# Optimization experiments

Hardware: AMD Instinct MI355X
Metric: run time of the kernel (lower is better)

Reference implementation:

```python
import jax, jax.numpy as jnp
import numpy as np

EMBED_DIM = 1024
NUM_HEADS = 16
HEAD_SIZE = EMBED_DIM // NUM_HEADS  # 64
MAX_EMBED_DIM = 2048
MAX_HEAD_SIZE = 128
B, T = 4, 2048


def setup_inputs() -> dict:
    key = jax.random.key(0)
    kx, kq, kk, kv = jax.random.split(key, 4)
    x = jax.random.normal(kx, (B, T, MAX_EMBED_DIM), dtype=jnp.float32)
    # base-head weights sized for the max config; slices are taken in reference()
    Wq = jax.random.normal(kq, (NUM_HEADS, MAX_HEAD_SIZE, MAX_EMBED_DIM), dtype=jnp.float32) * 0.02
    Wk = jax.random.normal(kk, (NUM_HEADS, MAX_HEAD_SIZE, MAX_EMBED_DIM), dtype=jnp.float32) * 0.02
    Wv = jax.random.normal(kv, (NUM_HEADS, MAX_HEAD_SIZE, MAX_EMBED_DIM), dtype=jnp.float32) * 0.02
    return {"x": x, "Wq": Wq, "Wk": Wk, "Wv": Wv}


def reference(x, Wq, Wk, Wv):
    Bx, Tx, _ = x.shape
    xs = x[:, :, :EMBED_DIM]                       # [B, T, E]
    # slice sampled sub-weights: [H, d, E]
    wq = Wq[:, :HEAD_SIZE, :EMBED_DIM]
    wk = Wk[:, :HEAD_SIZE, :EMBED_DIM]
    wv = Wv[:, :HEAD_SIZE, :EMBED_DIM]
    q = jnp.einsum('bte,hde->bhtd', xs, wq)        # [B, H, T, d]
    k = jnp.einsum('bte,hde->bhtd', xs, wk)
    v = jnp.einsum('bte,hde->bhtd', xs, wv)
    scale = jnp.asarray(HEAD_SIZE, x.dtype) ** -0.5
    wei = jnp.einsum('bhtd,bhsd->bhts', q, k) * scale   # [B, H, T, T]
    causal = jnp.tril(jnp.ones((Tx, Tx), dtype=bool))
    wei = jnp.where(causal, wei, jnp.asarray(-jnp.inf, wei.dtype))
    wei = jax.nn.softmax(wei, axis=-1)
    # dropout is identity in eval mode
    out = jnp.einsum('bhts,bhsd->bhtd', wei, v)    # [B, H, T, d]
    out = out.transpose(0, 2, 1, 3).reshape(Bx, Tx, NUM_HEADS * HEAD_SIZE)
    pad = MAX_EMBED_DIM - NUM_HEADS * HEAD_SIZE
    return jnp.pad(out, ((0, 0), (0, 0), (0, pad)))
```

## Files before the change

kernel.cpp:

```cpp
#include <hip/hip_runtime.h>

typedef __attribute__((ext_vector_type(8))) short bf16x8;
typedef __attribute__((ext_vector_type(4))) float f32x4;
typedef __attribute__((ext_vector_type(16))) float f32x16;
typedef __attribute__((ext_vector_type(8))) unsigned short u16x8;
typedef __attribute__((ext_vector_type(4))) unsigned int u32x4;

#define TT 2048

__device__ __forceinline__ unsigned short f2bf(float f) {
  unsigned int u = __builtin_bit_cast(unsigned int, f);
  u += 0x7FFFu + ((u >> 16) & 1u);
  return (unsigned short)(u >> 16);
}

__device__ __forceinline__ void gld16(const void* g, void* l) {
  __builtin_amdgcn_global_load_lds((const __attribute__((address_space(1))) void*)g,
                                   (__attribute__((address_space(3))) void*)l, 16, 0, 0);
}

__device__ __forceinline__ unsigned int cvtpk(float lo, float hi) {
  unsigned int r;
  asm("v_cvt_pk_bf16_f32 %0, %1, %2" : "=v"(r) : "v"(lo), "v"(hi));
  return r;
}

__device__ __forceinline__ void pl32swap(unsigned int& a, unsigned int& b) {
  asm volatile("v_permlane32_swap_b32 %0, %1" : "+v"(a), "+v"(b));
}

__global__ __launch_bounds__(256) void conv_x(const float* __restrict__ x,
                                              unsigned short* __restrict__ xb) {
  const size_t idx = ((size_t)blockIdx.x * 256 + threadIdx.x) * 8;
  const int m = (int)(idx >> 10);
  const int e = (int)(idx & 1023);
  const float4* s = (const float4*)(x + (size_t)m * 2048 + e);
  float4 a = s[0], b = s[1];
  u16x8 v;
  v[0]=f2bf(a.x); v[1]=f2bf(a.y); v[2]=f2bf(a.z); v[3]=f2bf(a.w);
  v[4]=f2bf(b.x); v[5]=f2bf(b.y); v[6]=f2bf(b.z); v[7]=f2bf(b.w);
  *(u16x8*)(xb + idx) = v;
}

__global__ __launch_bounds__(256) void conv_w(const float* __restrict__ Wq,
                                              const float* __restrict__ Wk,
                                              const float* __restrict__ Wv,
                                              unsigned short* __restrict__ wb) {
  const size_t idx = ((size_t)blockIdx.x * 256 + threadIdx.x) * 8;
  const int n = (int)(idx >> 10);
  const int e = (int)(idx & 1023);
  const int mat = n >> 10, hh = (n >> 6) & 15, d = n & 63;
  const float* W = (mat == 0) ? Wq : ((mat == 1) ? Wk : Wv);
  const float4* s = (const float4*)(W + ((size_t)hh * 128 + d) * 2048 + e);
  float4 a = s[0], b = s[1];
  u16x8 v;
  v[0]=f2bf(a.x); v[1]=f2bf(a.y); v[2]=f2bf(a.z); v[3]=f2bf(a.w);
  v[4]=f2bf(b.x); v[5]=f2bf(b.y); v[6]=f2bf(b.z); v[7]=f2bf(b.w);
  *(u16x8*)(wb + idx) = v;
}

__global__ __launch_bounds__(256) void qkv_gemm3(const unsigned short* __restrict__ xb,
                                                 const unsigned short* __restrict__ wb,
                                                 unsigned short* __restrict__ Q,
                                                 unsigned short* __restrict__ Kt,
                                                 unsigned short* __restrict__ Vt) {
  __shared__ unsigned short As[2][128 * 64];
  __shared__ unsigned short Bs[2][128 * 64];
  const int tid = threadIdx.x;
  const int w = tid >> 6, lane = tid & 63, g = lane >> 4, c = lane & 15;
  const int wm = w >> 1, wn = w & 1;
  const int m0 = blockIdx.x * 128;
  const int n0 = blockIdx.y * 128;

  f32x4 acc[4][4];
#pragma unroll
  for (int mi = 0; mi < 4; ++mi)
#pragma unroll
    for (int ni = 0; ni < 4; ++ni) acc[mi][ni] = (f32x4){0.f, 0.f, 0.f, 0.f};

  auto STAGE = [&](int t, int buf) {
    const int k0 = t * 64;
#pragma unroll
    for (int it = 0; it < 4; ++it) {
      const int o = (it * 256 + tid) * 16;
      const int r = o >> 7, cc = o & 127;
      const int cs = cc ^ ((r & 7) << 4);
      gld16(xb + ((size_t)(m0 + r) << 10) + k0 + (cs >> 1), (char*)&As[buf][0] + o);
      gld16(wb + ((size_t)(n0 + r) << 10) + k0 + (cs >> 1), (char*)&Bs[buf][0] + o);
    }
  };

  STAGE(0, 0);
  asm volatile("s_waitcnt vmcnt(0)" ::: "memory");
  __builtin_amdgcn_s_barrier();

  for (int t = 0; t < 16; ++t) {
    const int cur = t & 1;
    if (t + 1 < 16) STAGE(t + 1, cur ^ 1);
#pragma unroll
    for (int kk = 0; kk < 2; ++kk) {
      bf16x8 af[4], bfv[4];
#pragma unroll
      for (int mi = 0; mi < 4; ++mi) {
        const int r = wm * 64 + mi * 16 + c;
        const int cs = (kk * 64 + g * 16) ^ ((r & 7) << 4);
        af[mi] = *(const bf16x8*)((const char*)&As[cur][r * 64] + cs);
      }
#pragma unroll
      for (int ni = 0; ni < 4; ++ni) {
        const int r = wn * 64 + ni * 16 + c;
        const int cs = (kk * 64 + g * 16) ^ ((r & 7) << 4);
        bfv[ni] = *(const bf16x8*)((const char*)&Bs[cur][r * 64] + cs);
      }
      __builtin_amdgcn_s_setprio(1);
#pragma unroll
      for (int mi = 0; mi < 4; ++mi)
#pragma unroll
        for (int ni = 0; ni < 4; ++ni)
          acc[mi][ni] = __builtin_amdgcn_mfma_f32_16x16x32_bf16(af[mi], bfv[ni], acc[mi][ni], 0, 0, 0);
      __builtin_amdgcn_s_setprio(0);
    }
    asm volatile("s_waitcnt vmcnt(0)" ::: "memory");
    __builtin_amdgcn_s_barrier();
  }

#pragma unroll
  for (int mi = 0; mi < 4; ++mi) {
    const int row_l = wm * 64 + mi * 16 + g * 4;
#pragma unroll
    for (int i = 0; i < 4; ++i) {
      const int m = m0 + row_l + i;
      const int b = m >> 11, tt = m & 2047;
#pragma unroll
      for (int ni = 0; ni < 4; ++ni) {
        const int n = n0 + wn * 64 + ni * 16 + c;
        const int mat = n >> 10, hh = (n >> 6) & 15, d = n & 63;
        const unsigned short v = f2bf(acc[mi][ni][i]);
        const size_t bh = (size_t)(b * 16 + hh);
        if (mat == 0)      Q [(bh * TT + tt) * 64 + d] = v;
        else if (mat == 1) Kt[(bh * TT + tt) * 64 + d] = v;
        else               Vt[(bh * 64 + d) * TT + tt] = v;
      }
    }
  }
}

__global__ __launch_bounds__(256) void attn4(const unsigned short* __restrict__ Q,
                                             const unsigned short* __restrict__ K,
                                             const unsigned short* __restrict__ Vt,
                                             float* __restrict__ out) {
  __shared__ unsigned short Ks[2][4096];
  __shared__ unsigned short Vs[2][4096];
  const int blk = blockIdx.x;
  const int bh = blk & 63;
  const int qi = 15 - (blk >> 6);
  const int b = bh >> 4, h = bh & 15;
  const int tid = threadIdx.x;
  const int w = tid >> 6, lane = tid & 63;
  const int ql = lane & 31;
  const int hi = lane >> 5, hi8 = hi * 8;
  const int q0 = qi * 128;
  const int qw = q0 + w * 32;
  const int q = qw + ql;
  const unsigned short* Qp = Q  + (size_t)bh * TT * 64;
  const unsigned short* Kp = K  + (size_t)bh * TT * 64;
  const unsigned short* Vp = Vt + (size_t)bh * 64 * TT;

  bf16x8 qf0, qf1, qf2, qf3;
  {
    const unsigned short* qa = Qp + (size_t)q * 64 + hi8;
    qf0 = *(const bf16x8*)(qa);
    qf1 = *(const bf16x8*)(qa + 16);
    qf2 = *(const bf16x8*)(qa + 32);
    qf3 = *(const bf16x8*)(qa + 48);
  }

  f32x16 o0, o1;
#pragma unroll
  for (int r = 0; r < 16; ++r) { o0[r] = 0.f; o1[r] = 0.f; }
  float m = -3.0e38f, l = 0.f;
  const float c2 = 0.125f * 1.44269504f;

  const int nt = qi * 2 + 2;

  auto STAGE = [&](int t, int buf) {
#pragma unroll
    for (int it = 0; it < 2; ++it) {
      const int o = (it * 256 + tid) * 16;
      const int r = o >> 7, c = o & 127;
      const int cs = c ^ ((r & 7) << 4);
      gld16(Kp + (size_t)t * 4096 + r * 64 + (cs >> 1), (char*)&Ks[buf][0] + o);
      gld16(Vp + (size_t)r * 2048 + t * 64 + (cs >> 1), (char*)&Vs[buf][0] + o);
    }
  };

  STAGE(0, 0);
  asm volatile("s_waitcnt vmcnt(0)" ::: "memory");
  __syncthreads();

  int cur = 0;
  for (int t = 0; t < nt; ++t) {
    if (t + 1 < nt) STAGE(t + 1, cur ^ 1);

#pragma unroll
    for (int s = 0; s < 2; ++s) {
      const int ks32 = t * 64 + s * 32;
      if (ks32 <= qw) {
        const int krow = s * 32 + ql;
        const char* kb = (const char*)&Ks[cur][krow * 64];
        const int ksz = (krow & 7) << 4;
        bf16x8 kf0 = *(const bf16x8*)(kb + ((0  + hi * 16) ^ ksz));
        bf16x8 kf1 = *(const bf16x8*)(kb + ((32 + hi * 16) ^ ksz));
        bf16x8 kf2 = *(const bf16x8*)(kb + ((64 + hi * 16) ^ ksz));
        bf16x8 kf3 = *(const bf16x8*)(kb + ((96 + hi * 16) ^ ksz));
        const int vsz = (ql & 7) << 4;
        const char* vb0 = (const char*)&Vs[cur][ql * 64];
        const char* vb1 = (const char*)&Vs[cur][(ql + 32) * 64];
        bf16x8 vf0 = *(const bf16x8*)(vb0 + ((s * 64 + 0  + hi * 16) ^ vsz));
        bf16x8 vf1 = *(const bf16x8*)(vb0 + ((s * 64 + 32 + hi * 16) ^ vsz));
        bf16x8 vf2 = *(const bf16x8*)(vb1 + ((s * 64 + 0  + hi * 16) ^ vsz));
        bf16x8 vf3 = *(const bf16x8*)(vb1 + ((s * 64 + 32 + hi * 16) ^ vsz));

        f32x16 st;
#pragma unroll
        for (int r = 0; r < 16; ++r) st[r] = 0.f;
        __builtin_amdgcn_s_setprio(1);
        st = __builtin_amdgcn_mfma_f32_32x32x16_bf16(kf0, qf0, st, 0, 0, 0);
        st = __builtin_amdgcn_mfma_f32_32x32x16_bf16(kf1, qf1, st, 0, 0, 0);
        st = __builtin_amdgcn_mfma_f32_32x32x16_bf16(kf2, qf2, st, 0, 0, 0);
        st = __builtin_amdgcn_mfma_f32_32x32x16_bf16(kf3, qf3, st, 0, 0, 0);
        __builtin_amdgcn_s_setprio(0);

        if (ks32 == qw) {
#pragma unroll
          for (int r = 0; r < 16; ++r) {
            const int krw = (r & 3) + 8 * (r >> 2) + 4 * hi;
            if (krw > ql) st[r] = -3.0e38f;
          }
        }

        float t0 = fmaxf(st[0], st[1]),  t1 = fmaxf(st[2], st[3]);
        float t2 = fmaxf(st[4], st[5]),  t3 = fmaxf(st[6], st[7]);
        float t4 = fmaxf(st[8], st[9]),  t5 = fmaxf(st[10], st[11]);
        float t6 = fmaxf(st[12], st[13]), t7 = fmaxf(st[14], st[15]);
        t0 = fmaxf(t0, t1); t2 = fmaxf(t2, t3); t4 = fmaxf(t4, t5); t6 = fmaxf(t6, t7);
        float pm = fmaxf(fmaxf(t0, t2), fmaxf(t4, t6));
        pm = fmaxf(pm, __shfl_xor(pm, 32));
        if (!__all(pm - m <= 44.36f)) {
          const float mnew = fmaxf(m, pm);
          const float alpha = __builtin_amdgcn_exp2f((m - mnew) * c2);
          m = mnew;
          l *= alpha;
#pragma unroll
          for (int r = 0; r < 16; ++r) { o0[r] *= alpha; o1[r] *= alpha; }
        }
        float p[16];
        float rs = 0.f;
#pragma unroll
        for (int r = 0; r < 16; ++r) {
          p[r] = __builtin_amdgcn_exp2f((st[r] - m) * c2);
          rs += p[r];
        }
        rs += __shfl_xor(rs, 32);
        l += rs;

        unsigned int a0 = cvtpk(p[0], p[1]),  a1 = cvtpk(p[2], p[3]);
        unsigned int b0 = cvtpk(p[4], p[5]),  b1 = cvtpk(p[6], p[7]);
        pl32swap(a0, b0); pl32swap(a1, b1);
        unsigned int cc0 = cvtpk(p[8], p[9]),  cc1 = cvtpk(p[10], p[11]);
        unsigned int dd0 = cvtpk(p[12], p[13]), dd1 = cvtpk(p[14], p[15]);
        pl32swap(cc0, dd0); pl32swap(cc1, dd1);
        u32x4 pw0 = {a0, a1, b0, b1};
        u32x4 pw1 = {cc0, cc1, dd0, dd1};
        bf16x8 pf0 = __builtin_bit_cast(bf16x8, pw0);
        bf16x8 pf1 = __builtin_bit_cast(bf16x8, pw1);

        __builtin_amdgcn_s_setprio(1);
        o0 = __builtin_amdgcn_mfma_f32_32x32x16_bf16(vf0, pf0, o0, 0, 0, 0);
        o0 = __builtin_amdgcn_mfma_f32_32x32x16_bf16(vf1, pf1, o0, 0, 0, 0);
        o1 = __builtin_amdgcn_mfma_f32_32x32x16_bf16(vf2, pf0, o1, 0, 0, 0);
        o1 = __builtin_amdgcn_mfma_f32_32x32x16_bf16(vf3, pf1, o1, 0, 0, 0);
        __builtin_amdgcn_s_setprio(0);
      }
    }

    asm volatile("s_waitcnt vmcnt(0)" ::: "memory");
    __syncthreads();
    cur ^= 1;
  }

  const float inv = 1.f / l;
  float* ob = out + ((size_t)b * TT + q) * 2048 + h * 64;
#pragma unroll
  for (int r = 0; r < 16; ++r) {
    const int row = (r & 3) + 8 * (r >> 2) + 4 * hi;
    ob[row]      = o0[r] * inv;
    ob[32 + row] = o1[r] * inv;
  }

  const float4 z = make_float4(0.f, 0.f, 0.f, 0.f);
#pragma unroll
  for (int it = 0; it < 8; ++it) {
    const int idx = it * 256 + tid;
    const int r = idx >> 4, c4 = idx & 15;
    *((float4*)(out + ((size_t)b * TT + q0 + r) * 2048 + 1024 + h * 64) + c4) = z;
  }
}

extern "C" void kernel_launch(void* const* d_in, const int* in_sizes, int n_in,
                              void* d_out, int out_size, void* d_ws, size_t ws_size,
                              hipStream_t stream) {
  const float* x  = (const float*)d_in[0];
  const float* Wq = (const float*)d_in[1];
  const float* Wk = (const float*)d_in[2];
  const float* Wv = (const float*)d_in[3];

  unsigned short* wsp = (unsigned short*)d_ws;
  unsigned short* Q   = wsp;
  unsigned short* Kt  = wsp + (size_t)8388608;
  unsigned short* Vt  = wsp + (size_t)16777216;

  unsigned short* xb = (unsigned short*)d_out;
  unsigned short* wb = (unsigned short*)((char*)d_out + 33554432);
  float* out = (float*)d_out;

  conv_x<<<4096, 256, 0, stream>>>(x, xb);
  conv_w<<<1536, 256, 0, stream>>>(Wq, Wk, Wv, wb);
  qkv_gemm3<<<dim3(64, 24), 256, 0, stream>>>(xb, wb, Q, Kt, Vt);
  attn4<<<1024, 256, 0, stream>>>(Q, Kt, Vt, out);
}
```

Measured before the change: 167.4 us.

## Merge conversion kernels and halve GEMM K-tile to raise occupancy

```diff
diff --git a/kernel.cpp b/kernel.cpp
--- a/kernel.cpp
+++ b/kernel.cpp
@@ -29,64 +29,87 @@
   asm volatile("v_permlane32_swap_b32 %0, %1" : "+v"(a), "+v"(b));
 }
 
-__global__ __launch_bounds__(256) void conv_x(const float* __restrict__ x,
-                                              unsigned short* __restrict__ xb) {
-  const size_t idx = ((size_t)blockIdx.x * 256 + threadIdx.x) * 8;
-  const int m = (int)(idx >> 10);
-  const int e = (int)(idx & 1023);
-  const float4* s = (const float4*)(x + (size_t)m * 2048 + e);
+__global__ __launch_bounds__(256) void conv_all(const float* __restrict__ x,
+                                                const float* __restrict__ Wq,
+                                                const float* __restrict__ Wk,
+                                                const float* __restrict__ Wv,
+                                                unsigned short* __restrict__ xb,
+                                                unsigned short* __restrict__ wb) {
+  const int bid = blockIdx.x;
+  const float* src;
+  unsigned short* dst;
+  size_t idx;
+  if (bid < 4096) {
+    idx = ((size_t)bid * 256 + threadIdx.x) * 8;
+    const int m = (int)(idx >> 10);
+    const int e = (int)(idx & 1023);
+    src = x + (size_t)m * 2048 + e;
+    dst = xb + idx;
+  } else {
+    idx = ((size_t)(bid - 4096) * 256 + threadIdx.x) * 8;
+    const int n = (int)(idx >> 10);
+    const int e = (int)(idx & 1023);
+    const int mat = n >> 10, hh = (n >> 6) & 15, d = n & 63;
+    const float* W = (mat == 0) ? Wq : ((mat == 1) ? Wk : Wv);
+    src = W + ((size_t)hh * 128 + d) * 2048 + e;
+    dst = wb + idx;
+  }
+  const float4* s = (const float4*)src;
   float4 a = s[0], b = s[1];
   u16x8 v;
   v[0]=f2bf(a.x); v[1]=f2bf(a.y); v[2]=f2bf(a.z); v[3]=f2bf(a.w);
   v[4]=f2bf(b.x); v[5]=f2bf(b.y); v[6]=f2bf(b.z); v[7]=f2bf(b.w);
-  *(u16x8*)(xb + idx) = v;
-}
-
-__global__ __launch_bounds__(256) void conv_w(const float* __restrict__ Wq,
-                                              const float* __restrict__ Wk,
-                                              const float* __restrict__ Wv,
-                                              unsigned short* __restrict__ wb) {
-  const size_t idx = ((size_t)blockIdx.x * 256 + threadIdx.x) * 8;
-  const int n = (int)(idx >> 10);
-  const int e = (int)(idx & 1023);
-  const int mat = n >> 10, hh = (n >> 6) & 15, d = n & 63;
-  const float* W = (mat == 0) ? Wq : ((mat == 1) ? Wk : Wv);
-  const float4* s = (const float4*)(W + ((size_t)hh * 128 + d) * 2048 + e);
-  float4 a = s[0], b = s[1];
-  u16x8 v;
-  v[0]=f2bf(a.x); v[1]=f2bf(a.y); v[2]=f2bf(a.z); v[3]=f2bf(a.w);
-  v[4]=f2bf(b.x); v[5]=f2bf(b.y); v[6]=f2bf(b.z); v[7]=f2bf(b.w);
-  *(u16x8*)(wb + idx) = v;
-}
-
-__global__ __launch_bounds__(256) void qkv_gemm3(const unsigned short* __restrict__ xb,
-                                                 const unsigned short* __restrict__ wb,
-                                                 unsigned short* __restrict__ Q,
-                                                 unsigned short* __restrict__ Kt,
-                                                 unsigned short* __restrict__ Vt) {
-  __shared__ unsigned short As[2][128 * 64];
-  __shared__ unsigned short Bs[2][128 * 64];
+  *(u16x8*)dst = v;
+}
+
+__global__ __launch_bounds__(256, 4) void qkv_gemm4(const unsigned short* __restrict__ xb,
+                                                    const unsigned short* __restrict__ wb,
+                                                    unsigned short* __restrict__ Q,
+                                                    unsigned short* __restrict__ Kt,
+                                                    unsigned short* __restrict__ Vt) {
+  __shared__ unsigned short As[2][64 * 64];
+  __shared__ unsigned short Bs[2][64 * 64];
   const int tid = threadIdx.x;
   const int w = tid >> 6, lane = tid & 63, g = lane >> 4, c = lane & 15;
   const int wm = w >> 1, wn = w & 1;
   const int m0 = blockIdx.x * 128;
   const int n0 = blockIdx.y * 128;
 
+  size_t aoff[2], boff[2];
+  int lofs[2];
+#pragma unroll
+  for (int it = 0; it < 2; ++it) {
+    const int o = (it * 256 + tid) * 16;
+    const int row = o >> 7, stored = o & 127;
+    const int logical = stored ^ ((row & 7) << 4);
+    const int seg = logical >> 6, kb = logical & 63;
+    const int m = row + (seg << 6);
+    aoff[it] = ((size_t)(m0 + m) << 10) + (kb >> 1);
+    boff[it] = ((size_t)(n0 + m) << 10) + (kb >> 1);
+    lofs[it] = o;
+  }
+  int ardo[4], brdo[4];
+#pragma unroll
+  for (int mi = 0; mi < 4; ++mi) {
+    const int m = wm * 64 + mi * 16 + c;
+    const int row = m & 63, seg = m >> 6;
+    ardo[mi] = row * 128 + (((seg << 6) + (g << 4)) ^ ((row & 7) << 4));
+    const int n = wn * 64 + mi * 16 + c;
+    const int nrow = n & 63, nseg = n >> 6;
+    brdo[mi] = nrow * 128 + (((nseg << 6) + (g << 4)) ^ ((nrow & 7) << 4));
+  }
+
   f32x4 acc[4][4];
 #pragma unroll
   for (int mi = 0; mi < 4; ++mi)
 #pragma unroll
     for (int ni = 0; ni < 4; ++ni) acc[mi][ni] = (f32x4){0.f, 0.f, 0.f, 0.f};
 
-  auto STAGE = [&](int t, int buf) {
-    const int k0 = t * 64;
-#pragma unroll
-    for (int it = 0; it < 4; ++it) {
-      const int o = (it * 256 + tid) * 16;
-      const int r = o >> 7, cc = o & 127;
-      const int cs = cc ^ ((r & 7) << 4);
-      gld16(xb + ((size_t)(m0 + r) << 10) + k0 + (cs >> 1), (char*)&As[buf][0] + o);
-      gld16(wb + ((size_t)(n0 + r) << 10) + k0 + (cs >> 1), (char*)&Bs[buf][0] + o);
+  auto STAGE = [&](int k0, int buf) {
+#pragma unroll
+    for (int it = 0; it < 2; ++it) {
+      gld16(xb + aoff[it] + k0, (char*)&As[buf][0] + lofs[it]);
+      gld16(wb + boff[it] + k0, (char*)&Bs[buf][0] + lofs[it]);
     }
   };
 
@@ -94,32 +117,22 @@
   asm volatile("s_waitcnt vmcnt(0)" ::: "memory");
   __builtin_amdgcn_s_barrier();
 
-  for (int t = 0; t < 16; ++t) {
+  for (int t = 0; t < 32; ++t) {
     const int cur = t & 1;
-    if (t + 1 < 16) STAGE(t + 1, cur ^ 1);
-#pragma unroll
-    for (int kk = 0; kk < 2; ++kk) {
-      bf16x8 af[4], bfv[4];
-#pragma unroll
-      for (int mi = 0; mi < 4; ++mi) {
-        const int r = wm * 64 + mi * 16 + c;
-        const int cs = (kk * 64 + g * 16) ^ ((r & 7) << 4);
-        af[mi] = *(const bf16x8*)((const char*)&As[cur][r * 64] + cs);
-      }
-#pragma unroll
-      for (int ni = 0; ni < 4; ++ni) {
-        const int r = wn * 64 + ni * 16 + c;
-        const int cs = (kk * 64 + g * 16) ^ ((r & 7) << 4);
-        bfv[ni] = *(const bf16x8*)((const char*)&Bs[cur][r * 64] + cs);
-      }
-      __builtin_amdgcn_s_setprio(1);
-#pragma unroll
-      for (int mi = 0; mi < 4; ++mi)
-#pragma unroll
-        for (int ni = 0; ni < 4; ++ni)
-          acc[mi][ni] = __builtin_amdgcn_mfma_f32_16x16x32_bf16(af[mi], bfv[ni], acc[mi][ni], 0, 0, 0);
-      __builtin_amdgcn_s_setprio(0);
-    }
+    if (t + 1 < 32) STAGE((t + 1) * 32, cur ^ 1);
+    bf16x8 af[4], bfv[4];
+#pragma unroll
+    for (int mi = 0; mi < 4; ++mi) {
+      af[mi]  = *(const bf16x8*)((const char*)&As[cur][0] + ardo[mi]);
+      bfv[mi] = *(const bf16x8*)((const char*)&Bs[cur][0] + brdo[mi]);
+    }
+    __builtin_amdgcn_s_setprio(1);
+#pragma unroll
+    for (int mi = 0; mi < 4; ++mi)
+#pragma unroll
+      for (int ni = 0; ni < 4; ++ni)
+        acc[mi][ni] = __builtin_amdgcn_mfma_f32_16x16x32_bf16(af[mi], bfv[ni], acc[mi][ni], 0, 0, 0);
+    __builtin_amdgcn_s_setprio(0);
     asm volatile("s_waitcnt vmcnt(0)" ::: "memory");
     __builtin_amdgcn_s_barrier();
   }
@@ -324,8 +337,7 @@
   unsigned short* wb = (unsigned short*)((char*)d_out + 33554432);
   float* out = (float*)d_out;
 
-  conv_x<<<4096, 256, 0, stream>>>(x, xb);
-  conv_w<<<1536, 256, 0, stream>>>(Wq, Wk, Wv, wb);
-  qkv_gemm3<<<dim3(64, 24), 256, 0, stream>>>(xb, wb, Q, Kt, Vt);
+  conv_all<<<5632, 256, 0, stream>>>(x, Wq, Wk, Wv, xb, wb);
+  qkv_gemm4<<<dim3(64, 24), 256, 0, stream>>>(xb, wb, Q, Kt, Vt);
   attn4<<<1024, 256, 0, stream>>>(Q, Kt, Vt, out);
 }
```

Result: no change. 167.0 us (-0.2%).
